# Optimization experiments

Hardware: AMD Instinct MI355X
Metric: run time of the kernel (lower is better)

The kernel has to match this reference:

```python
import jax, jax.numpy as jnp
import numpy as np

B, L, E, H = 8, 1024, 1024, 16
D = E // H
EPS = 1e-5


def setup_inputs() -> dict:
    key = jax.random.key(0)
    ks = jax.random.split(key, 3)
    s = 1.0 / np.sqrt(E)
    return {
        "x": jax.random.normal(ks[0], (B, L, E), dtype=jnp.float32),
        "w_qkv": jax.random.normal(ks[1], (3 * E, E), dtype=jnp.float32) * s,
        "b_qkv": jnp.zeros((3 * E,), dtype=jnp.float32),
        "w_out": jax.random.normal(ks[2], (E, E), dtype=jnp.float32) * s,
        "b_out": jnp.zeros((E,), dtype=jnp.float32),
        "gamma": jnp.ones((E,), dtype=jnp.float32),
        "beta": jnp.zeros((E,), dtype=jnp.float32),
    }


def reference(x, w_qkv, b_qkv, w_out, b_out, gamma, beta):
    # Packed QKV projection (torch nn.MultiheadAttention in_proj): (B,L,3E)
    qkv = jnp.einsum("ble,fe->blf", x, w_qkv) + b_qkv
    q, k, v = jnp.split(qkv, 3, axis=-1)
    # (B,L,H,D)
    q = q.reshape(B, L, H, D) * (1.0 / np.sqrt(D))
    k = k.reshape(B, L, H, D)
    v = v.reshape(B, L, H, D)
    scores = jnp.einsum("blhd,bmhd->bhlm", q, k)           # (B,H,L,L)
    w = jax.nn.softmax(scores, axis=-1)                     # (B,H,L,L)
    ctx = jnp.einsum("bhlm,bmhd->blhd", w, v).reshape(B, L, E)
    attn_out = jnp.einsum("ble,fe->blf", ctx, w_out) + b_out
    # Residual + LayerNorm
    h = x + attn_out
    mu = h.mean(axis=-1, keepdims=True)
    var = ((h - mu) ** 2).mean(axis=-1, keepdims=True)
    hn = (h - mu) * jax.lax.rsqrt(var + EPS) * gamma + beta
    pooled = hn.mean(axis=1)                                # (B,E)
    # torch returns head-averaged weights (B,L,L); then mean over query dim
    avg_attn = w.mean(axis=1).mean(axis=1)                  # (B,L)
    return pooled, avg_attn
```

## Files before the change

kernel.cpp:

```cpp
#include <hip/hip_runtime.h>
#include <math.h>

constexpr int Bc = 8;
constexpr int Lc = 1024;
constexpr int Ec = 1024;
constexpr int Hc = 16;
constexpr int Dc = 64;
constexpr float EPSc = 1e-5f;

typedef _Float16 f16;
typedef f16 half8 __attribute__((ext_vector_type(8)));
typedef float floatx4 __attribute__((ext_vector_type(4)));

static __device__ inline void gload_lds16(const f16* g, f16* l) {
    __builtin_amdgcn_global_load_lds(
        (const __attribute__((address_space(1))) void*)g,
        (__attribute__((address_space(3))) void*)l, 16, 0, 0);
}

static __device__ inline void cvt_body(const float* __restrict__ src,
                                       f16* __restrict__ dst, int n8,
                                       int blk, int nblk) {
    int i = blk * 256 + threadIdx.x;
    const int stride = nblk * 256;
    for (; i < n8; i += stride) {
        float4 a = *(const float4*)(src + (size_t)i * 8);
        float4 b = *(const float4*)(src + (size_t)i * 8 + 4);
        half8 p;
        p[0] = (f16)a.x; p[1] = (f16)a.y; p[2] = (f16)a.z; p[3] = (f16)a.w;
        p[4] = (f16)b.x; p[5] = (f16)b.y; p[6] = (f16)b.z; p[7] = (f16)b.w;
        *(half8*)(dst + (size_t)i * 8) = p;
    }
}

__global__ __launch_bounds__(256)
void cvt3_kernel(const float* __restrict__ x, const float* __restrict__ wq,
                 const float* __restrict__ wo, f16* __restrict__ xh,
                 f16* __restrict__ wqh, f16* __restrict__ woh) {
    const int b = blockIdx.x;
    if (b < 2048)       cvt_body(x,  xh,  (Bc * Lc * Ec) / 8, b, 2048);
    else if (b < 3584)  cvt_body(wq, wqh, (3 * Ec * Ec) / 8, b - 2048, 1536);
    else                cvt_body(wo, woh, (Ec * Ec) / 8, b - 3584, 512);
}

__global__ __launch_bounds__(256)
void gemm_nt_h(const f16* __restrict__ A, const f16* __restrict__ Bm,
               const float* __restrict__ bias, float* __restrict__ Cf,
               f16* __restrict__ Ch, int M, int N, int K) {
    constexpr int TILE = 128;
    constexpr int KT = 64;
    constexpr int RSs = 64;
    __shared__ __align__(16) f16 As[TILE * RSs];
    __shared__ __align__(16) f16 Bs[TILE * RSs];

    const int tid = threadIdx.x;
    const int bm = blockIdx.x * TILE;
    const int bn = blockIdx.y * TILE;

    const int wave = tid >> 6;
    const int lane = tid & 63;
    const int wm = (wave >> 1) * 64;
    const int wn = (wave & 1) * 64;
    const int r16 = lane & 15;
    const int kg = lane >> 4;
    const int kx = r16 & 7;

    floatx4 acc[4][4];
#pragma unroll
    for (int i = 0; i < 4; ++i)
#pragma unroll
        for (int j = 0; j < 4; ++j) acc[i][j] = (floatx4){0.f, 0.f, 0.f, 0.f};

    const int rbase = tid >> 3;
    const int kcg = (tid & 7) ^ (rbase & 7);
    const f16* apt = A + (size_t)(bm + rbase) * K + kcg * 8;
    const f16* bpt = Bm + (size_t)(bn + rbase) * K + kcg * 8;
    f16* asl = As + tid * 8;
    f16* bsl = Bs + tid * 8;

    for (int k0 = 0; k0 < K; k0 += KT) {
        __syncthreads();
#pragma unroll
        for (int q = 0; q < 4; ++q) {
            gload_lds16(apt + (size_t)(q * 32) * K + k0, asl + q * 2048);
            gload_lds16(bpt + (size_t)(q * 32) * K + k0, bsl + q * 2048);
        }
        __syncthreads();

#pragma unroll
        for (int ks = 0; ks < 2; ++ks) {
            const int kslot = ((ks * 4 + kg) ^ kx) * 8;
            half8 af[4], bf[4];
#pragma unroll
            for (int i = 0; i < 4; ++i)
                af[i] = *(const half8*)&As[(wm + 16 * i + r16) * RSs + kslot];
#pragma unroll
            for (int j = 0; j < 4; ++j)
                bf[j] = *(const half8*)&Bs[(wn + 16 * j + r16) * RSs + kslot];
#pragma unroll
            for (int i = 0; i < 4; ++i)
#pragma unroll
                for (int j = 0; j < 4; ++j)
                    acc[i][j] = __builtin_amdgcn_mfma_f32_16x16x32_f16(af[i], bf[j], acc[i][j], 0, 0, 0);
        }
    }

    if (Ch) {
#pragma unroll
        for (int j = 0; j < 4; ++j) {
            const int col = bn + wn + 16 * j + r16;
            const float bv = bias[col];
#pragma unroll
            for (int i = 0; i < 4; ++i) {
                const int row0e = bm + wm + 16 * i + kg * 4;
#pragma unroll
                for (int r = 0; r < 4; ++r)
                    Ch[(size_t)(row0e + r) * N + col] = (f16)(acc[i][j][r] + bv);
            }
        }
    } else {
#pragma unroll
        for (int j = 0; j < 4; ++j) {
            const int col = bn + wn + 16 * j + r16;
            const float bv = bias[col];
#pragma unroll
            for (int i = 0; i < 4; ++i) {
                const int row0e = bm + wm + 16 * i + kg * 4;
#pragma unroll
                for (int r = 0; r < 4; ++r)
                    Cf[(size_t)(row0e + r) * N + col] = acc[i][j][r] + bv;
            }
        }
    }
}

constexpr int AQT = 128;
constexpr int AKT = 128;
constexpr int ANT = Lc / AKT;
constexpr int AKP = 72;
constexpr int AWP = 136;
constexpr int AVP = 136;

constexpr int AQ_OFF  = 0;
constexpr int AKV_OFF = 4608;
constexpr int AW_OFF  = AKV_OFF + 4608;
constexpr int ARS_OFF = AW_OFF + 8704;
constexpr int ACOL_OFF = ARS_OFF + 128;
constexpr int ASMEM   = ACOL_OFF + 1024;

__global__ __launch_bounds__(256, 2)
void attn_kernel(const f16* __restrict__ qkv, f16* __restrict__ ctx,
                 float* __restrict__ avg_out) {
    __shared__ __align__(16) float smemf[ASMEM];
    f16* Kq = (f16*)(smemf + AQ_OFF);
    f16* Kt = (f16*)(smemf + AKV_OFF);
    f16* Vt = (f16*)(smemf + AKV_OFF);
    f16* WS = (f16*)(smemf + AW_OFF);
    float* RS  = smemf + ARS_OFF;
    float* COL = smemf + ACOL_OFF;

    const int tid = threadIdx.x;
    const int h = blockIdx.x, qt = blockIdx.y, b = blockIdx.z;
    const int l0 = qt * AQT;
    const size_t rowstride = 3 * Ec;
    const f16* base = qkv + (size_t)b * Lc * rowstride + (size_t)h * Dc;

    const int wave = tid >> 6, lane = tid & 63;
    const int r16 = lane & 15, kg = lane >> 4;
    const int wm = (wave >> 1) * 64;
    const int wn = (wave & 1) * 64;

    if (tid < 128) RS[tid] = 0.f;
#pragma unroll
    for (int t = 0; t < 4; ++t) COL[t * 256 + tid] = 0.f;

    const int srow = tid >> 1;
    const int sh = (tid & 1) * 32;

    {
        const f16* src = base + (size_t)(l0 + srow) * rowstride + sh;
        f16* dst = Kq + srow * AKP + sh;
#pragma unroll
        for (int jj = 0; jj < 4; ++jj) {
            half8 p = *(const half8*)(src + jj * 8);
#pragma unroll
            for (int e = 0; e < 8; ++e) p[e] = p[e] * (f16)0.125f;
            *(half8*)(dst + jj * 8) = p;
        }
    }

    const f16* kstage = base + (size_t)srow * rowstride + Ec + sh;
    half8 kreg[4];
#pragma unroll
    for (int jj = 0; jj < 4; ++jj) kreg[jj] = *(const half8*)(kstage + jj * 8);

    float rs[4][4];
#pragma unroll
    for (int i = 0; i < 4; ++i)
#pragma unroll
        for (int r = 0; r < 4; ++r) rs[i][r] = 0.f;

    for (int kt = 0; kt < ANT; ++kt) {
        __syncthreads();
        {
            f16* dst = Kt + srow * AKP + sh;
#pragma unroll
            for (int jj = 0; jj < 4; ++jj)
                *(half8*)(dst + jj * 8) = kreg[jj];
        }
        if (kt + 1 < ANT) {
            const f16* src = kstage + (size_t)((kt + 1) * AKT) * rowstride;
#pragma unroll
            for (int jj = 0; jj < 4; ++jj) kreg[jj] = *(const half8*)(src + jj * 8);
        }
        __syncthreads();

        floatx4 s[4][4];
#pragma unroll
        for (int i = 0; i < 4; ++i)
#pragma unroll
            for (int j = 0; j < 4; ++j) s[i][j] = (floatx4){0.f, 0.f, 0.f, 0.f};
#pragma unroll
        for (int ks = 0; ks < 2; ++ks) {
            half8 af[4], bf[4];
#pragma unroll
            for (int i = 0; i < 4; ++i)
                af[i] = *(const half8*)&Kq[(wm + 16 * i + r16) * AKP + ks * 32 + kg * 8];
#pragma unroll
            for (int j = 0; j < 4; ++j)
                bf[j] = *(const half8*)&Kt[(wn + 16 * j + r16) * AKP + ks * 32 + kg * 8];
#pragma unroll
            for (int i = 0; i < 4; ++i)
#pragma unroll
                for (int j = 0; j < 4; ++j)
                    s[i][j] = __builtin_amdgcn_mfma_f32_16x16x32_f16(af[i], bf[j], s[i][j], 0, 0, 0);
        }
#pragma unroll
        for (int i = 0; i < 4; ++i)
#pragma unroll
            for (int r = 0; r < 4; ++r)
                rs[i][r] += __expf(s[i][0][r]) + __expf(s[i][1][r]) +
                            __expf(s[i][2][r]) + __expf(s[i][3][r]);
    }

#pragma unroll
    for (int jj = 0; jj < 4; ++jj) kreg[jj] = *(const half8*)(kstage + jj * 8);

#pragma unroll
    for (int i = 0; i < 4; ++i)
#pragma unroll
        for (int r = 0; r < 4; ++r) {
            float v = rs[i][r];
            v += __shfl_xor(v, 1); v += __shfl_xor(v, 2);
            v += __shfl_xor(v, 4); v += __shfl_xor(v, 8);
            rs[i][r] = v;
        }
    if (r16 == 0) {
#pragma unroll
        for (int i = 0; i < 4; ++i)
#pragma unroll
            for (int r = 0; r < 4; ++r)
                atomicAdd(&RS[wm + 16 * i + 4 * kg + r], rs[i][r]);
    }
    __syncthreads();
    if (tid < 128) RS[tid] = 1.0f / RS[tid];
    __syncthreads();

    float rinv[4][4];
#pragma unroll
    for (int i = 0; i < 4; ++i)
#pragma unroll
        for (int r = 0; r < 4; ++r) rinv[i][r] = RS[wm + 16 * i + 4 * kg + r];

    floatx4 cacc[2][4];
#pragma unroll
    for (int p = 0; p < 2; ++p)
#pragma unroll
        for (int j = 0; j < 4; ++j) cacc[p][j] = (floatx4){0.f, 0.f, 0.f, 0.f};
    const int qb = wave * 32;

    for (int kt = 0; kt < ANT; ++kt) {
        __syncthreads();
        {
            f16* dst = Kt + srow * AKP + sh;
#pragma unroll
            for (int jj = 0; jj < 4; ++jj)
                *(half8*)(dst + jj * 8) = kreg[jj];
        }
        half8 vreg[4];
        {
            const f16* src = base + (size_t)(kt * AKT + srow) * rowstride + 2 * Ec + sh;
#pragma unroll
            for (int jj = 0; jj < 4; ++jj) vreg[jj] = *(const half8*)(src + jj * 8);
        }
        if (kt + 1 < ANT) {
            const f16* src = kstage + (size_t)((kt + 1) * AKT) * rowstride;
#pragma unroll
            for (int jj = 0; jj < 4; ++jj) kreg[jj] = *(const half8*)(src + jj * 8);
        }
        __syncthreads();

        floatx4 s[4][4];
#pragma unroll
        for (int i = 0; i < 4; ++i)
#pragma unroll
            for (int j = 0; j < 4; ++j) s[i][j] = (floatx4){0.f, 0.f, 0.f, 0.f};
#pragma unroll
        for (int ks = 0; ks < 2; ++ks) {
            half8 af[4], bf[4];
#pragma unroll
            for (int i = 0; i < 4; ++i)
                af[i] = *(const half8*)&Kq[(wm + 16 * i + r16) * AKP + ks * 32 + kg * 8];
#pragma unroll
            for (int j = 0; j < 4; ++j)
                bf[j] = *(const half8*)&Kt[(wn + 16 * j + r16) * AKP + ks * 32 + kg * 8];
#pragma unroll
            for (int i = 0; i < 4; ++i)
#pragma unroll
                for (int j = 0; j < 4; ++j)
                    s[i][j] = __builtin_amdgcn_mfma_f32_16x16x32_f16(af[i], bf[j], s[i][j], 0, 0, 0);
        }

        float cs[4] = {0.f, 0.f, 0.f, 0.f};
#pragma unroll
        for (int i = 0; i < 4; ++i)
#pragma unroll
            for (int j = 0; j < 4; ++j)
#pragma unroll
                for (int r = 0; r < 4; ++r) {
                    float w = __expf(s[i][j][r]) * rinv[i][r];
                    s[i][j][r] = w;
                    cs[j] += w;
                }

        __syncthreads();

#pragma unroll
        for (int i = 0; i < 4; ++i)
#pragma unroll
            for (int r = 0; r < 4; ++r) {
                f16* wrow = WS + (wm + 16 * i + 4 * kg + r) * AWP + wn + r16;
#pragma unroll
                for (int j = 0; j < 4; ++j) wrow[16 * j] = (f16)s[i][j][r];
            }

#pragma unroll
        for (int jj = 0; jj < 4; ++jj) {
#pragma unroll
            for (int e = 0; e < 8; ++e)
                Vt[(sh + jj * 8 + e) * AVP + srow] = vreg[jj][e];
        }

#pragma unroll
        for (int j = 0; j < 4; ++j) {
            float c = cs[j];
            c += __shfl_xor(c, 16);
            c += __shfl_xor(c, 32);
            if (kg == 0) atomicAdd(&COL[kt * AKT + wn + 16 * j + r16], c);
        }

        __syncthreads();

#pragma unroll
        for (int ks2 = 0; ks2 < 4; ++ks2) {
            half8 wa[2], vb[4];
#pragma unroll
            for (int p = 0; p < 2; ++p)
                wa[p] = *(const half8*)&WS[(qb + 16 * p + r16) * AWP + ks2 * 32 + kg * 8];
#pragma unroll
            for (int j = 0; j < 4; ++j)
                vb[j] = *(const half8*)&Vt[(16 * j + r16) * AVP + ks2 * 32 + kg * 8];
#pragma unroll
            for (int p = 0; p < 2; ++p)
#pragma unroll
                for (int j = 0; j < 4; ++j)
                    cacc[p][j] = __builtin_amdgcn_mfma_f32_16x16x32_f16(wa[p], vb[j], cacc[p][j], 0, 0, 0);
        }
    }

#pragma unroll
    for (int p = 0; p < 2; ++p)
#pragma unroll
        for (int r = 0; r < 4; ++r) {
            f16* dst = ctx + (size_t)(b * Lc + l0 + qb + 16 * p + 4 * kg + r) * Ec + h * Dc + r16;
#pragma unroll
            for (int j = 0; j < 4; ++j) dst[16 * j] = (f16)cacc[p][j][r];
        }

    __syncthreads();
#pragma unroll
    for (int t = 0; t < 4; ++t) {
        int m = t * 256 + tid;
        atomicAdd(&avg_out[b * Lc + m], COL[m] * (1.0f / (Hc * Lc)));
    }
}

__global__ __launch_bounds__(256)
void stats_kernel(const float* __restrict__ x, const float* __restrict__ attn_out,
                  float2* __restrict__ stats) {
    const int row = blockIdx.x;
    const int tid = threadIdx.x;
    const float* xp = x + (size_t)row * Ec;
    const float* ap = attn_out + (size_t)row * Ec;
    float4 xv = *(const float4*)(xp + tid * 4);
    float4 av = *(const float4*)(ap + tid * 4);
    float h0 = xv.x + av.x, h1 = xv.y + av.y, h2 = xv.z + av.z, h3 = xv.w + av.w;
    float s = h0 + h1 + h2 + h3;
    float ss = h0 * h0 + h1 * h1 + h2 * h2 + h3 * h3;
#pragma unroll
    for (int off = 32; off; off >>= 1) {
        s += __shfl_xor(s, off);
        ss += __shfl_xor(ss, off);
    }
    __shared__ float wsum[4], wsq[4];
    const int wave = tid >> 6, lane = tid & 63;
    if (lane == 0) { wsum[wave] = s; wsq[wave] = ss; }
    __syncthreads();
    if (tid == 0) {
        float ts = wsum[0] + wsum[1] + wsum[2] + wsum[3];
        float tq = wsq[0] + wsq[1] + wsq[2] + wsq[3];
        float mean = ts * (1.0f / Ec);
        float var = tq * (1.0f / Ec) - mean * mean;
        stats[row] = make_float2(mean, rsqrtf(var + EPSc));
    }
}

__global__ __launch_bounds__(256)
void pool_kernel(const float* __restrict__ x, const float* __restrict__ attn_out,
                 const float2* __restrict__ stats, const float* __restrict__ gamma,
                 const float* __restrict__ beta, float* __restrict__ pooled) {
    const int b = blockIdx.z;
    const int f = blockIdx.y * 256 + threadIdx.x;
    const int l0 = blockIdx.x * 64;
    const float g = gamma[f];
    const float be = beta[f];
    float acc = 0.f;
    for (int l = l0; l < l0 + 64; ++l) {
        size_t idx = (size_t)(b * Lc + l) * Ec + f;
        float2 st = stats[b * Lc + l];
        float h = x[idx] + attn_out[idx];
        acc += (h - st.x) * st.y * g + be;
    }
    atomicAdd(&pooled[b * Ec + f], acc * (1.0f / Lc));
}

extern "C" void kernel_launch(void* const* d_in, const int* in_sizes, int n_in,
                              void* d_out, int out_size, void* d_ws, size_t ws_size,
                              hipStream_t stream) {
    const float* x      = (const float*)d_in[0];
    const float* w_qkv  = (const float*)d_in[1];
    const float* b_qkv  = (const float*)d_in[2];
    const float* w_out  = (const float*)d_in[3];
    const float* b_out  = (const float*)d_in[4];
    const float* gamma  = (const float*)d_in[5];
    const float* beta   = (const float*)d_in[6];
    float* out = (float*)d_out;

    f16* wsh = (f16*)d_ws;
    f16* qkv_h  = wsh;
    f16* ctx_h  = qkv_h + (size_t)25165824;
    f16* x_h    = ctx_h + (size_t)8388608;
    f16* wqkv_h = x_h + (size_t)8388608;
    f16* wout_h = wqkv_h + (size_t)3145728;
    float* attn_out = (float*)(wout_h + (size_t)1048576);
    float* stats = attn_out + (size_t)8388608;

    const int M = Bc * Lc;

    hipMemsetAsync(d_out, 0, (size_t)out_size * sizeof(float), stream);

    cvt3_kernel<<<4096, 256, 0, stream>>>(x, w_qkv, w_out, x_h, wqkv_h, wout_h);

    dim3 g1(M / 128, (3 * Ec) / 128);
    gemm_nt_h<<<g1, 256, 0, stream>>>(x_h, wqkv_h, b_qkv, nullptr, qkv_h, M, 3 * Ec, Ec);

    dim3 g2(Hc, Lc / AQT, Bc);
    attn_kernel<<<g2, 256, 0, stream>>>(qkv_h, ctx_h, out + Bc * Ec);

    dim3 g3(M / 128, Ec / 128);
    gemm_nt_h<<<g3, 256, 0, stream>>>(ctx_h, wout_h, b_out, attn_out, nullptr, M, Ec, Ec);

    stats_kernel<<<M, 256, 0, stream>>>(x, attn_out, (float2*)stats);

    dim3 g5(16, 4, Bc);
    pool_kernel<<<g5, 256, 0, stream>>>(x, attn_out, (float2*)stats, gamma, beta, out);
}
```

Baseline: 310.9 us.

## Fuse residual add and LayerNorm row statistics into output-projection GEMM epilogue

The output-projection GEMM epilogue now adds the residual x, stores h, and accumulates per-row sum and sum-of-squares through shuffles and atomics into a partial buffer. The separate stats kernel becomes a tiny finalize kernel, and the pool kernel reads h directly instead of re-reading x and attn_out. This removes one full pass over two 32MB tensors and cuts pool reads in half. The cost is an extra memset, a residual load in the epilogue, and atomics, with ordering nondeterminism in the sums.

```diff
diff --git a/kernel.cpp b/kernel.cpp
--- a/kernel.cpp
+++ b/kernel.cpp
@@ -45,7 +45,8 @@
 
 __global__ __launch_bounds__(256)
 void gemm_nt_h(const f16* __restrict__ A, const f16* __restrict__ Bm,
-               const float* __restrict__ bias, float* __restrict__ Cf,
+               const float* __restrict__ bias, const float* __restrict__ resid,
+               float* __restrict__ spart, float* __restrict__ Cf,
                f16* __restrict__ Ch, int M, int N, int K) {
     constexpr int TILE = 128;
     constexpr int KT = 64;
@@ -119,6 +120,11 @@
             }
         }
     } else {
+        float rsum[4][4], rsq[4][4];
+#pragma unroll
+        for (int i = 0; i < 4; ++i)
+#pragma unroll
+            for (int r = 0; r < 4; ++r) { rsum[i][r] = 0.f; rsq[i][r] = 0.f; }
 #pragma unroll
         for (int j = 0; j < 4; ++j) {
             const int col = bn + wn + 16 * j + r16;
@@ -127,9 +133,32 @@
             for (int i = 0; i < 4; ++i) {
                 const int row0e = bm + wm + 16 * i + kg * 4;
 #pragma unroll
-                for (int r = 0; r < 4; ++r)
-                    Cf[(size_t)(row0e + r) * N + col] = acc[i][j][r] + bv;
+                for (int r = 0; r < 4; ++r) {
+                    const size_t idx = (size_t)(row0e + r) * N + col;
+                    float v = acc[i][j][r] + bv;
+                    if (resid) v += resid[idx];
+                    Cf[idx] = v;
+                    rsum[i][r] += v;
+                    rsq[i][r] += v * v;
+                }
             }
+        }
+        if (spart) {
+#pragma unroll
+            for (int i = 0; i < 4; ++i)
+#pragma unroll
+                for (int r = 0; r < 4; ++r) {
+                    float s = rsum[i][r], q = rsq[i][r];
+                    s += __shfl_xor(s, 1); s += __shfl_xor(s, 2);
+                    s += __shfl_xor(s, 4); s += __shfl_xor(s, 8);
+                    q += __shfl_xor(q, 1); q += __shfl_xor(q, 2);
+                    q += __shfl_xor(q, 4); q += __shfl_xor(q, 8);
+                    if (r16 == 0) {
+                        const int row = bm + wm + 16 * i + kg * 4 + r;
+                        atomicAdd(&spart[2 * row], s);
+                        atomicAdd(&spart[2 * row + 1], q);
+                    }
+                }
         }
     }
 }
@@ -396,39 +425,19 @@
 }
 
 __global__ __launch_bounds__(256)
-void stats_kernel(const float* __restrict__ x, const float* __restrict__ attn_out,
-                  float2* __restrict__ stats) {
-    const int row = blockIdx.x;
-    const int tid = threadIdx.x;
-    const float* xp = x + (size_t)row * Ec;
-    const float* ap = attn_out + (size_t)row * Ec;
-    float4 xv = *(const float4*)(xp + tid * 4);
-    float4 av = *(const float4*)(ap + tid * 4);
-    float h0 = xv.x + av.x, h1 = xv.y + av.y, h2 = xv.z + av.z, h3 = xv.w + av.w;
-    float s = h0 + h1 + h2 + h3;
-    float ss = h0 * h0 + h1 * h1 + h2 * h2 + h3 * h3;
-#pragma unroll
-    for (int off = 32; off; off >>= 1) {
-        s += __shfl_xor(s, off);
-        ss += __shfl_xor(ss, off);
-    }
-    __shared__ float wsum[4], wsq[4];
-    const int wave = tid >> 6, lane = tid & 63;
-    if (lane == 0) { wsum[wave] = s; wsq[wave] = ss; }
-    __syncthreads();
-    if (tid == 0) {
-        float ts = wsum[0] + wsum[1] + wsum[2] + wsum[3];
-        float tq = wsq[0] + wsq[1] + wsq[2] + wsq[3];
-        float mean = ts * (1.0f / Ec);
-        float var = tq * (1.0f / Ec) - mean * mean;
-        stats[row] = make_float2(mean, rsqrtf(var + EPSc));
-    }
+void stats_fin_kernel(const float* __restrict__ spart, float2* __restrict__ stats) {
+    const int row = blockIdx.x * 256 + threadIdx.x;
+    float ts = spart[2 * row];
+    float tq = spart[2 * row + 1];
+    float mean = ts * (1.0f / Ec);
+    float var = tq * (1.0f / Ec) - mean * mean;
+    stats[row] = make_float2(mean, rsqrtf(var + EPSc));
 }
 
 __global__ __launch_bounds__(256)
-void pool_kernel(const float* __restrict__ x, const float* __restrict__ attn_out,
-                 const float2* __restrict__ stats, const float* __restrict__ gamma,
-                 const float* __restrict__ beta, float* __restrict__ pooled) {
+void pool_kernel(const float* __restrict__ hbuf, const float2* __restrict__ stats,
+                 const float* __restrict__ gamma, const float* __restrict__ beta,
+                 float* __restrict__ pooled) {
     const int b = blockIdx.z;
     const int f = blockIdx.y * 256 + threadIdx.x;
     const int l0 = blockIdx.x * 64;
@@ -438,8 +447,7 @@
     for (int l = l0; l < l0 + 64; ++l) {
         size_t idx = (size_t)(b * Lc + l) * Ec + f;
         float2 st = stats[b * Lc + l];
-        float h = x[idx] + attn_out[idx];
-        acc += (h - st.x) * st.y * g + be;
+        acc += (hbuf[idx] - st.x) * st.y * g + be;
     }
     atomicAdd(&pooled[b * Ec + f], acc * (1.0f / Lc));
 }
@@ -462,26 +470,30 @@
     f16* x_h    = ctx_h + (size_t)8388608;
     f16* wqkv_h = x_h + (size_t)8388608;
     f16* wout_h = wqkv_h + (size_t)3145728;
-    float* attn_out = (float*)(wout_h + (size_t)1048576);
-    float* stats = attn_out + (size_t)8388608;
+    float* hbuf  = (float*)(wout_h + (size_t)1048576);
+    float* stats = hbuf + (size_t)8388608;
+    float* spart = stats + (size_t)16384;
 
     const int M = Bc * Lc;
 
     hipMemsetAsync(d_out, 0, (size_t)out_size * sizeof(float), stream);
+    hipMemsetAsync(spart, 0, (size_t)2 * M * sizeof(float), stream);
 
     cvt3_kernel<<<4096, 256, 0, stream>>>(x, w_qkv, w_out, x_h, wqkv_h, wout_h);
 
     dim3 g1(M / 128, (3 * Ec) / 128);
-    gemm_nt_h<<<g1, 256, 0, stream>>>(x_h, wqkv_h, b_qkv, nullptr, qkv_h, M, 3 * Ec, Ec);
+    gemm_nt_h<<<g1, 256, 0, stream>>>(x_h, wqkv_h, b_qkv, nullptr, nullptr,
+                                      nullptr, qkv_h, M, 3 * Ec, Ec);
 
     dim3 g2(Hc, Lc / AQT, Bc);
     attn_kernel<<<g2, 256, 0, stream>>>(qkv_h, ctx_h, out + Bc * Ec);
 
     dim3 g3(M / 128, Ec / 128);
-    gemm_nt_h<<<g3, 256, 0, stream>>>(ctx_h, wout_h, b_out, attn_out, nullptr, M, Ec, Ec);
-
-    stats_kernel<<<M, 256, 0, stream>>>(x, attn_out, (float2*)stats);
+    gemm_nt_h<<<g3, 256, 0, stream>>>(ctx_h, wout_h, b_out, x, spart,
+                                      hbuf, nullptr, M, Ec, Ec);
+
+    stats_fin_kernel<<<M / 256, 256, 0, stream>>>(spart, (float2*)stats);
 
     dim3 g5(16, 4, Bc);
-    pool_kernel<<<g5, 256, 0, stream>>>(x, attn_out, (float2*)stats, gamma, beta, out);
-}
+    pool_kernel<<<g5, 256, 0, stream>>>(hbuf, (float2*)stats, gamma, beta, out);
+}
```

Result: slower. 318.1 us, median of 2 (+2.3%).
